# Performance work log

Hardware: AMD Instinct MI355X
Metric: run time of the kernel (lower is better)

## Reference

```python
import jax, jax.numpy as jnp
import numpy as np

S = 2048      # sequence length (q_seq == kv_seq, self-attention)
D = 1024      # hidden_size
H = 16        # num_heads
DH = D // H   # per-head dim
LN_EPS = 1e-5


def setup_inputs() -> dict:
    key = jax.random.key(0)
    ks = jax.random.split(key, 8)
    init = lambda k, shape: (jax.random.normal(k, shape, dtype=jnp.float32)
                             / np.float32(np.sqrt(shape[-1])))
    return {
        "x": jax.random.normal(ks[0], (S, D), dtype=jnp.float32),
        "logit_bias": jax.random.normal(ks[1], (S, H * S), dtype=jnp.float32) * 0.1,
        "mask": jax.random.bernoulli(ks[2], 0.9, (S, S)),
        "Wq": init(ks[3], (D, D)),
        "Wk": init(ks[4], (D, D)),
        "Wv": init(ks[5], (D, D)),
        "Wo": init(ks[6], (D, D)),
        "ln_w": jnp.ones((D,), dtype=jnp.float32),
        "ln_b": jnp.zeros((D,), dtype=jnp.float32),
    }


def reference(x, logit_bias, mask, Wq, Wk, Wv, Wo, ln_w, ln_b):
    # Projections (eqx.nn.Linear: y = W @ x, no bias), split into heads.
    q = (x @ Wq.T).reshape(S, H, DH)  # [s,h,d]
    k = (x @ Wk.T).reshape(S, H, DH)  # [S,h,d]
    v = (x @ Wv.T).reshape(S, H, DH)  # [S,h,d]

    # Scaled scores + per-head additive logit bias.
    scale = jnp.asarray(1.0 / np.sqrt(DH), dtype=q.dtype)
    logits = jnp.einsum('shd,Shd->hsS', q * scale, k)  # [h,s,S]
    logits = logits + logit_bias.reshape(S, H, S).transpose(1, 0, 2)

    # Boolean mask (q_seq, kv_seq) broadcast over heads.
    logits = jnp.where(mask[None, :, :], logits, jnp.finfo(logits.dtype).min)

    # Stable softmax in float32 (matches result_type promotion in source).
    weights = jax.nn.softmax(logits.astype(jnp.float32), axis=-1).astype(logits.dtype)

    attn = jnp.einsum('hsS,Shd->shd', weights, v).reshape(S, D)
    attn_out = attn @ Wo.T  # output projection, no bias

    # Residual + LayerNorm over last dim (eqx.nn.LayerNorm, eps=1e-5).
    res = attn_out + x
    mean = jnp.mean(res, axis=-1, keepdims=True)
    var = jnp.var(res, axis=-1, keepdims=True)
    normed = (res - mean) * jax.lax.rsqrt(var + LN_EPS)
    return normed * ln_w + ln_b
```

## Files before the change

### kernel.cpp

```cpp
#include <hip/hip_runtime.h>

#define SS 2048
#define DD 1024
#define HH 16
#define DHD 64
#define HSN (HH * SS)
#define LOG2E 1.44269504088896340736f

typedef __bf16 bf16x8 __attribute__((ext_vector_type(8)));
typedef __bf16 bf16x4 __attribute__((ext_vector_type(4)));
typedef float f32x4 __attribute__((ext_vector_type(4)));
typedef unsigned int u32;
typedef unsigned long long u64;

__device__ __forceinline__ void glds16(const void* g, void* l) {
  __builtin_amdgcn_global_load_lds(
      (const __attribute__((address_space(1))) u32*)(const u32*)g,
      (__attribute__((address_space(3))) u32*)(u32*)l, 16, 0, 0);
}

__global__ __launch_bounds__(256) void cvt_all_kernel(const float* __restrict__ x,
                                                      const float* __restrict__ Wq,
                                                      const float* __restrict__ Wk,
                                                      const float* __restrict__ Wv,
                                                      const float* __restrict__ Wo,
                                                      __bf16* xb, __bf16* Wqb, __bf16* Wkb,
                                                      __bf16* Wvb, __bf16* Wob) {
  const int z = blockIdx.z;
  const int n4 = (z == 0 ? SS * DD : DD * DD) / 4;
  const int i = blockIdx.x * 256 + threadIdx.x;
  if (i >= n4) return;
  const float* in = z == 0 ? x : (z == 1 ? Wq : (z == 2 ? Wk : (z == 3 ? Wv : Wo)));
  __bf16* out = z == 0 ? xb : (z == 1 ? Wqb : (z == 2 ? Wkb : (z == 3 ? Wvb : Wob)));
  const float4 v = ((const float4*)in)[i];
  bf16x4 r;
  r[0] = (__bf16)v.x; r[1] = (__bf16)v.y; r[2] = (__bf16)v.z; r[3] = (__bf16)v.w;
  *(bf16x4*)&out[(long)i * 4] = r;
}

__global__ __launch_bounds__(256) void pack_mask(const int* __restrict__ mask,
                                                 u64* __restrict__ mp) {
  const long i = (long)blockIdx.x * 256 + threadIdx.x;
  const u64 b = __ballot(mask[i] != 0);
  if ((threadIdx.x & 63) == 0) mp[i >> 6] = b;
}

template <int BM>
__device__ __forceinline__ void gemm_body(const __bf16* __restrict__ A,
                                          const __bf16* __restrict__ B,
                                          void* __restrict__ Cout, float scale, int mode) {
  constexpr int MR = BM / 32;
  __shared__ alignas(16) __bf16 As[BM * 32];
  __shared__ alignas(16) __bf16 Bs[128 * 32];
  const int tid = threadIdx.x;
  const int lane = tid & 63;
  const int wave = tid >> 6;
  const long m0 = (long)blockIdx.y * BM;
  const long n0 = (long)blockIdx.x * 128;
  const int wm = (wave >> 1) * (BM / 2);
  const int wn = (wave & 1) * 64;
  const int g = lane >> 4, r16 = lane & 15;
  const int srow = tid >> 2, sseg = (tid & 3) * 8;

  f32x4 acc[MR][4] = {};

  for (int k0 = 0; k0 < DD; k0 += 32) {
#pragma unroll
    for (int it = 0; it < 2; ++it) {
      const int row = srow + it * 64;
      glds16(&B[(n0 + row) * DD + k0 + sseg], &Bs[row * 32 + sseg]);
    }
#pragma unroll
    for (int it = 0; it < BM / 64; ++it) {
      const int row = srow + it * 64;
      glds16(&A[(m0 + row) * DD + k0 + sseg], &As[row * 32 + sseg]);
    }
    __syncthreads();
    bf16x8 af[MR], bfr[4];
#pragma unroll
    for (int r = 0; r < MR; ++r) af[r] = *(const bf16x8*)&As[(wm + r * 16 + r16) * 32 + g * 8];
#pragma unroll
    for (int c = 0; c < 4; ++c) bfr[c] = *(const bf16x8*)&Bs[(wn + c * 16 + r16) * 32 + g * 8];
#pragma unroll
    for (int r = 0; r < MR; ++r)
#pragma unroll
      for (int c = 0; c < 4; ++c)
        acc[r][c] = __builtin_amdgcn_mfma_f32_16x16x32_bf16(af[r], bfr[c], acc[r][c], 0, 0, 0);
    __syncthreads();
  }

  if (mode == 2) {
#pragma unroll
    for (int r = 0; r < MR; ++r)
#pragma unroll
      for (int c = 0; c < 4; ++c) {
        const long row0 = m0 + wm + r * 16 + g * 4;
        const long col = n0 + wn + c * 16 + r16;
        bf16x4 rv;
#pragma unroll
        for (int i = 0; i < 4; ++i) rv[i] = (__bf16)(acc[r][c][i] * scale);
        *(bf16x4*)&((__bf16*)Cout)[col * SS + row0] = rv;
      }
  } else {
#pragma unroll
    for (int r = 0; r < MR; ++r)
#pragma unroll
      for (int c = 0; c < 4; ++c)
#pragma unroll
        for (int i = 0; i < 4; ++i) {
          const long row = m0 + wm + r * 16 + g * 4 + i;
          const long col = n0 + wn + c * 16 + r16;
          const float v = acc[r][c][i] * scale;
          if (mode == 1) ((float*)Cout)[row * DD + col] = v;
          else           ((__bf16*)Cout)[row * DD + col] = (__bf16)v;
        }
  }
}

__global__ __launch_bounds__(256) void gemm_qkv(const __bf16* __restrict__ A,
                                                const __bf16* __restrict__ B0,
                                                const __bf16* __restrict__ B1,
                                                const __bf16* __restrict__ B2,
                                                __bf16* C0, __bf16* C1, __bf16* C2,
                                                float s0) {
  const int z = blockIdx.z;
  const __bf16* B = z == 0 ? B0 : (z == 1 ? B1 : B2);
  __bf16* C = z == 0 ? C0 : (z == 1 ? C1 : C2);
  gemm_body<128>(A, B, C, z == 0 ? s0 : 1.0f, z == 2 ? 2 : 0);
}

__global__ __launch_bounds__(256) void gemm_o(const __bf16* __restrict__ A,
                                              const __bf16* __restrict__ B,
                                              float* __restrict__ C) {
  gemm_body<64>(A, B, C, 1.0f, 1);
}

__global__ __launch_bounds__(256) void attn_kernel(
    const __bf16* __restrict__ Q, const __bf16* __restrict__ K,
    const __bf16* __restrict__ Vt, const float* __restrict__ bias,
    const u64* __restrict__ mp, __bf16* __restrict__ Aout) {
  __shared__ alignas(16) __bf16 Ks[64][72];
  __shared__ alignas(16) __bf16 Vts[64][72];
  __shared__ alignas(16) __bf16 Ps[4][16][72];
  const int tid = threadIdx.x;
  const int lane = tid & 63;
  const int wave = tid >> 6;
  const int h = blockIdx.y;
  const int q0 = blockIdx.x * 64 + wave * 16;
  const int g = lane >> 4, r16 = lane & 15;
  const int myq = q0 + r16;
  const int srow = tid >> 2;

  bf16x8 qf[2];
#pragma unroll
  for (int c = 0; c < 2; ++c)
    qf[c] = *(const bf16x8*)&Q[(long)myq * DD + h * DHD + c * 32 + g * 8];

  const float* bp = &bias[(long)myq * HSN + h * SS];
  const u64* mrow_p = &mp[(long)myq * (SS / 64)];

  f32x4 o[4] = {};
  float mrow = -__builtin_inff();
  float lsum = 0.f;

  for (int kv0 = 0; kv0 < SS; kv0 += 64) {
    __syncthreads();
#pragma unroll
    for (int it = 0; it < 2; ++it) {
      const int seg = (tid & 3) + it * 4;
      *(bf16x8*)&Ks[srow][seg * 8] =
          *(const bf16x8*)&K[(long)(kv0 + srow) * DD + h * DHD + seg * 8];
      *(bf16x8*)&Vts[srow][seg * 8] =
          *(const bf16x8*)&Vt[(long)(h * DHD + srow) * SS + kv0 + seg * 8];
    }

    float4 bv[4];
#pragma unroll
    for (int t = 0; t < 4; ++t) bv[t] = *(const float4*)&bp[kv0 + t * 16 + g * 4];
    const u64 mw = mrow_p[kv0 >> 6];
    __syncthreads();

    f32x4 s[4];
#pragma unroll
    for (int t = 0; t < 4; ++t) {
      bf16x8 kf0 = *(const bf16x8*)&Ks[t * 16 + r16][g * 8];
      bf16x8 kf1 = *(const bf16x8*)&Ks[t * 16 + r16][32 + g * 8];
      f32x4 acc = {};
      acc = __builtin_amdgcn_mfma_f32_16x16x32_bf16(kf0, qf[0], acc, 0, 0, 0);
      s[t] = __builtin_amdgcn_mfma_f32_16x16x32_bf16(kf1, qf[1], acc, 0, 0, 0);
    }

    float sv[4][4];
#pragma unroll
    for (int t = 0; t < 4; ++t) {
      const u32 mb = (u32)(mw >> (t * 16 + g * 4));
      sv[t][0] = (mb & 1u) ? s[t][0] + bv[t].x * LOG2E : -1e38f;
      sv[t][1] = (mb & 2u) ? s[t][1] + bv[t].y * LOG2E : -1e38f;
      sv[t][2] = (mb & 4u) ? s[t][2] + bv[t].z * LOG2E : -1e38f;
      sv[t][3] = (mb & 8u) ? s[t][3] + bv[t].w * LOG2E : -1e38f;
    }

    float m4 = -1e38f;
#pragma unroll
    for (int t = 0; t < 4; ++t)
#pragma unroll
      for (int i = 0; i < 4; ++i) m4 = fmaxf(m4, sv[t][i]);
    m4 = fmaxf(m4, __shfl_xor(m4, 16));
    m4 = fmaxf(m4, __shfl_xor(m4, 32));
    const float mnew = fmaxf(mrow, m4);
    const float alpha = exp2f(mrow - mnew);
    float ps = 0.f;
    float p[4][4];
#pragma unroll
    for (int t = 0; t < 4; ++t)
#pragma unroll
      for (int i = 0; i < 4; ++i) {
        p[t][i] = exp2f(sv[t][i] - mnew);
        ps += p[t][i];
      }
    ps += __shfl_xor(ps, 16);
    ps += __shfl_xor(ps, 32);
    lsum = lsum * alpha + ps;
    mrow = mnew;
#pragma unroll
    for (int db = 0; db < 4; ++db) o[db] *= alpha;

#pragma unroll
    for (int t = 0; t < 4; ++t) {
      bf16x4 pb;
#pragma unroll
      for (int i = 0; i < 4; ++i) pb[i] = (__bf16)p[t][i];
      *(bf16x4*)&Ps[wave][r16][t * 16 + g * 4] = pb;
    }

#pragma unroll
    for (int kh = 0; kh < 2; ++kh) {
      bf16x8 pf = *(const bf16x8*)&Ps[wave][r16][kh * 32 + g * 8];
#pragma unroll
      for (int db = 0; db < 4; ++db) {
        bf16x8 vf = *(const bf16x8*)&Vts[db * 16 + r16][kh * 32 + g * 8];
        o[db] = __builtin_amdgcn_mfma_f32_16x16x32_bf16(vf, pf, o[db], 0, 0, 0);
      }
    }
  }

  const float rn = 1.f / lsum;
#pragma unroll
  for (int db = 0; db < 4; ++db) {
    bf16x4 r;
#pragma unroll
    for (int i = 0; i < 4; ++i) r[i] = (__bf16)(o[db][i] * rn);
    *(bf16x4*)&Aout[(long)myq * DD + h * DHD + db * 16 + g * 4] = r;
  }
}

__global__ __launch_bounds__(256) void ln_kernel(const float* __restrict__ attn_out,
                                                 const float* __restrict__ x,
                                                 const float* __restrict__ w,
                                                 const float* __restrict__ b,
                                                 float* __restrict__ out) {
  const long row = blockIdx.x;
  const int tid = threadIdx.x;
  float v[4];
  float s = 0.f, s2 = 0.f;
#pragma unroll
  for (int j = 0; j < 4; ++j) {
    const int d = tid + j * 256;
    const float r = attn_out[row * DD + d] + x[row * DD + d];
    v[j] = r; s += r; s2 += r * r;
  }
#pragma unroll
  for (int off = 1; off < 64; off <<= 1) {
    s  += __shfl_xor(s, off);
    s2 += __shfl_xor(s2, off);
  }
  __shared__ float ss[4], ss2[4];
  if ((tid & 63) == 0) { ss[tid >> 6] = s; ss2[tid >> 6] = s2; }
  __syncthreads();
  s = ss[0] + ss[1] + ss[2] + ss[3];
  s2 = ss2[0] + ss2[1] + ss2[2] + ss2[3];
  const float mean = s * (1.f / DD);
  const float var = s2 * (1.f / DD) - mean * mean;
  const float inv = rsqrtf(var + 1e-5f);
#pragma unroll
  for (int j = 0; j < 4; ++j) {
    const int d = tid + j * 256;
    out[row * DD + d] = (v[j] - mean) * inv * w[d] + b[d];
  }
}

extern "C" void kernel_launch(void* const* d_in, const int* in_sizes, int n_in,
                              void* d_out, int out_size, void* d_ws, size_t ws_size,
                              hipStream_t stream) {
  const float* x    = (const float*)d_in[0];
  const float* bias = (const float*)d_in[1];
  const int*   mask = (const int*)d_in[2];
  const float* Wq   = (const float*)d_in[3];
  const float* Wk   = (const float*)d_in[4];
  const float* Wv   = (const float*)d_in[5];
  const float* Wo   = (const float*)d_in[6];
  const float* lnw  = (const float*)d_in[7];
  const float* lnb  = (const float*)d_in[8];
  float* out = (float*)d_out;

  char* ws = (char*)d_ws;
  const size_t MB = 1024 * 1024;
  __bf16* xb   = (__bf16*)(ws + 0);
  __bf16* Wqb  = (__bf16*)(ws + 4 * MB);
  __bf16* Wkb  = (__bf16*)(ws + 6 * MB);
  __bf16* Wvb  = (__bf16*)(ws + 8 * MB);
  __bf16* Wob  = (__bf16*)(ws + 10 * MB);
  __bf16* Qb   = (__bf16*)(ws + 12 * MB);
  __bf16* Kb   = (__bf16*)(ws + 16 * MB);
  __bf16* Vtb  = (__bf16*)(ws + 24 * MB);
  __bf16* Atnb = (__bf16*)(ws + 28 * MB);
  float*  AOut = (float*)(ws + 32 * MB);
  u64*    mpk  = (u64*)(ws + 40 * MB);

  cvt_all_kernel<<<dim3(SS * DD / 1024, 1, 5), dim3(256), 0, stream>>>(
      x, Wq, Wk, Wv, Wo, xb, Wqb, Wkb, Wvb, Wob);

  pack_mask<<<dim3(SS * SS / 256), dim3(256), 0, stream>>>(mask, mpk);

  gemm_qkv<<<dim3(DD / 128, SS / 128, 3), dim3(256), 0, stream>>>(
      xb, Wqb, Wkb, Wvb, Qb, Kb, Vtb, 0.125f * LOG2E);

  attn_kernel<<<dim3(SS / 64, HH), dim3(256), 0, stream>>>(Qb, Kb, Vtb, bias, mpk, Atnb);

  gemm_o<<<dim3(DD / 128, SS / 64), dim3(256), 0, stream>>>(Atnb, Wob, AOut);

  ln_kernel<<<dim3(SS), dim3(256), 0, stream>>>(AOut, x, lnw, lnb, out);
}
```

Before: 488.0 us.

## Widen attention KV tile, remap blocks across XCDs, vectorize layernorm

Attention now processes 128 KV columns per iteration instead of 64, which halves the number of loop iterations and barriers and loads more bias per step. The GEMM and attention kernels remap the flat block index so consecutive blocks spread across the chiplets (XCD-aware swizzle), which is meant to improve L2 locality. The layernorm kernel switches to float4 loads and stores. These changes raise register pressure and LDS use in attention, which may lower occupancy.

```diff
diff --git a/kernel.cpp b/kernel.cpp
--- a/kernel.cpp
+++ b/kernel.cpp
@@ -48,15 +48,16 @@
 template <int BM>
 __device__ __forceinline__ void gemm_body(const __bf16* __restrict__ A,
                                           const __bf16* __restrict__ B,
-                                          void* __restrict__ Cout, float scale, int mode) {
+                                          void* __restrict__ Cout, float scale, int mode,
+                                          int bx, int by) {
   constexpr int MR = BM / 32;
   __shared__ alignas(16) __bf16 As[BM * 32];
   __shared__ alignas(16) __bf16 Bs[128 * 32];
   const int tid = threadIdx.x;
   const int lane = tid & 63;
   const int wave = tid >> 6;
-  const long m0 = (long)blockIdx.y * BM;
-  const long n0 = (long)blockIdx.x * 128;
+  const long m0 = (long)by * BM;
+  const long n0 = (long)bx * 128;
   const int wm = (wave >> 1) * (BM / 2);
   const int wn = (wave & 1) * 64;
   const int g = lane >> 4, r16 = lane & 15;
@@ -123,33 +124,42 @@
                                                 const __bf16* __restrict__ B2,
                                                 __bf16* C0, __bf16* C1, __bf16* C2,
                                                 float s0) {
-  const int z = blockIdx.z;
+  const int flat = blockIdx.x + 8 * (blockIdx.y + 16 * blockIdx.z);
+  const int flat2 = (flat & 7) * 48 + (flat >> 3);
+  const int bx = flat2 & 7;
+  const int t = flat2 >> 3;
+  const int by = t & 15;
+  const int z = t >> 4;
   const __bf16* B = z == 0 ? B0 : (z == 1 ? B1 : B2);
   __bf16* C = z == 0 ? C0 : (z == 1 ? C1 : C2);
-  gemm_body<128>(A, B, C, z == 0 ? s0 : 1.0f, z == 2 ? 2 : 0);
+  gemm_body<128>(A, B, C, z == 0 ? s0 : 1.0f, z == 2 ? 2 : 0, bx, by);
 }
 
 __global__ __launch_bounds__(256) void gemm_o(const __bf16* __restrict__ A,
                                               const __bf16* __restrict__ B,
                                               float* __restrict__ C) {
-  gemm_body<64>(A, B, C, 1.0f, 1);
+  const int flat = blockIdx.x + 8 * blockIdx.y;
+  const int flat2 = (flat & 7) * 32 + (flat >> 3);
+  gemm_body<64>(A, B, C, 1.0f, 1, flat2 & 7, flat2 >> 3);
 }
 
 __global__ __launch_bounds__(256) void attn_kernel(
     const __bf16* __restrict__ Q, const __bf16* __restrict__ K,
     const __bf16* __restrict__ Vt, const float* __restrict__ bias,
     const u64* __restrict__ mp, __bf16* __restrict__ Aout) {
-  __shared__ alignas(16) __bf16 Ks[64][72];
-  __shared__ alignas(16) __bf16 Vts[64][72];
-  __shared__ alignas(16) __bf16 Ps[4][16][72];
+  __shared__ alignas(16) __bf16 Ks[128][72];
+  __shared__ alignas(16) __bf16 Vts[64][136];
+  __shared__ alignas(16) __bf16 Ps[4][16][136];
   const int tid = threadIdx.x;
   const int lane = tid & 63;
   const int wave = tid >> 6;
-  const int h = blockIdx.y;
-  const int q0 = blockIdx.x * 64 + wave * 16;
+  const int flat = blockIdx.x + 32 * blockIdx.y;
+  const int flat2 = (flat & 7) * 64 + (flat >> 3);
+  const int bx = flat2 & 31;
+  const int h = flat2 >> 5;
+  const int q0 = bx * 64 + wave * 16;
   const int g = lane >> 4, r16 = lane & 15;
   const int myq = q0 + r16;
-  const int srow = tid >> 2;
 
   bf16x8 qf[2];
 #pragma unroll
@@ -163,26 +173,30 @@
   float mrow = -__builtin_inff();
   float lsum = 0.f;
 
-  for (int kv0 = 0; kv0 < SS; kv0 += 64) {
+  const int krow = tid >> 1, kcb = (tid & 1) * 4;
+  const int vrow = tid >> 2, vcb = tid & 3;
+
+  for (int kv0 = 0; kv0 < SS; kv0 += 128) {
     __syncthreads();
 #pragma unroll
-    for (int it = 0; it < 2; ++it) {
-      const int seg = (tid & 3) + it * 4;
-      *(bf16x8*)&Ks[srow][seg * 8] =
-          *(const bf16x8*)&K[(long)(kv0 + srow) * DD + h * DHD + seg * 8];
-      *(bf16x8*)&Vts[srow][seg * 8] =
-          *(const bf16x8*)&Vt[(long)(h * DHD + srow) * SS + kv0 + seg * 8];
-    }
-
-    float4 bv[4];
-#pragma unroll
-    for (int t = 0; t < 4; ++t) bv[t] = *(const float4*)&bp[kv0 + t * 16 + g * 4];
-    const u64 mw = mrow_p[kv0 >> 6];
+    for (int it = 0; it < 4; ++it)
+      *(bf16x8*)&Ks[krow][(kcb + it) * 8] =
+          *(const bf16x8*)&K[(long)(kv0 + krow) * DD + h * DHD + (kcb + it) * 8];
+#pragma unroll
+    for (int it = 0; it < 4; ++it)
+      *(bf16x8*)&Vts[vrow][(vcb + it * 4) * 8] =
+          *(const bf16x8*)&Vt[(long)(h * DHD + vrow) * SS + kv0 + (vcb + it * 4) * 8];
+
+    float4 bv[8];
+#pragma unroll
+    for (int t = 0; t < 8; ++t) bv[t] = *(const float4*)&bp[kv0 + t * 16 + g * 4];
+    const u64 mwA = mrow_p[kv0 >> 6];
+    const u64 mwB = mrow_p[(kv0 >> 6) + 1];
     __syncthreads();
 
-    f32x4 s[4];
-#pragma unroll
-    for (int t = 0; t < 4; ++t) {
+    f32x4 s[8];
+#pragma unroll
+    for (int t = 0; t < 8; ++t) {
       bf16x8 kf0 = *(const bf16x8*)&Ks[t * 16 + r16][g * 8];
       bf16x8 kf1 = *(const bf16x8*)&Ks[t * 16 + r16][32 + g * 8];
       f32x4 acc = {};
@@ -190,33 +204,32 @@
       s[t] = __builtin_amdgcn_mfma_f32_16x16x32_bf16(kf1, qf[1], acc, 0, 0, 0);
     }
 
-    float sv[4][4];
-#pragma unroll
-    for (int t = 0; t < 4; ++t) {
-      const u32 mb = (u32)(mw >> (t * 16 + g * 4));
-      sv[t][0] = (mb & 1u) ? s[t][0] + bv[t].x * LOG2E : -1e38f;
-      sv[t][1] = (mb & 2u) ? s[t][1] + bv[t].y * LOG2E : -1e38f;
-      sv[t][2] = (mb & 4u) ? s[t][2] + bv[t].z * LOG2E : -1e38f;
-      sv[t][3] = (mb & 8u) ? s[t][3] + bv[t].w * LOG2E : -1e38f;
+    float l[8][4];
+#pragma unroll
+    for (int t = 0; t < 8; ++t) {
+      const u32 mb = (u32)((t < 4 ? mwA : mwB) >> ((t & 3) * 16 + g * 4));
+      l[t][0] = (mb & 1u) ? s[t][0] + bv[t].x * LOG2E : -1e38f;
+      l[t][1] = (mb & 2u) ? s[t][1] + bv[t].y * LOG2E : -1e38f;
+      l[t][2] = (mb & 4u) ? s[t][2] + bv[t].z * LOG2E : -1e38f;
+      l[t][3] = (mb & 8u) ? s[t][3] + bv[t].w * LOG2E : -1e38f;
     }
 
     float m4 = -1e38f;
 #pragma unroll
-    for (int t = 0; t < 4; ++t)
-#pragma unroll
-      for (int i = 0; i < 4; ++i) m4 = fmaxf(m4, sv[t][i]);
+    for (int t = 0; t < 8; ++t)
+#pragma unroll
+      for (int i = 0; i < 4; ++i) m4 = fmaxf(m4, l[t][i]);
     m4 = fmaxf(m4, __shfl_xor(m4, 16));
     m4 = fmaxf(m4, __shfl_xor(m4, 32));
     const float mnew = fmaxf(mrow, m4);
     const float alpha = exp2f(mrow - mnew);
     float ps = 0.f;
-    float p[4][4];
-#pragma unroll
-    for (int t = 0; t < 4; ++t)
+#pragma unroll
+    for (int t = 0; t < 8; ++t)
 #pragma unroll
       for (int i = 0; i < 4; ++i) {
-        p[t][i] = exp2f(sv[t][i] - mnew);
-        ps += p[t][i];
+        l[t][i] = exp2f(l[t][i] - mnew);
+        ps += l[t][i];
       }
     ps += __shfl_xor(ps, 16);
     ps += __shfl_xor(ps, 32);
@@ -226,15 +239,15 @@
     for (int db = 0; db < 4; ++db) o[db] *= alpha;
 
 #pragma unroll
-    for (int t = 0; t < 4; ++t) {
+    for (int t = 0; t < 8; ++t) {
       bf16x4 pb;
 #pragma unroll
-      for (int i = 0; i < 4; ++i) pb[i] = (__bf16)p[t][i];
+      for (int i = 0; i < 4; ++i) pb[i] = (__bf16)l[t][i];
       *(bf16x4*)&Ps[wave][r16][t * 16 + g * 4] = pb;
     }
 
 #pragma unroll
-    for (int kh = 0; kh < 2; ++kh) {
+    for (int kh = 0; kh < 4; ++kh) {
       bf16x8 pf = *(const bf16x8*)&Ps[wave][r16][kh * 32 + g * 8];
 #pragma unroll
       for (int db = 0; db < 4; ++db) {
@@ -261,14 +274,12 @@
                                                  float* __restrict__ out) {
   const long row = blockIdx.x;
   const int tid = threadIdx.x;
-  float v[4];
+  const float4 a4 = ((const float4*)&attn_out[row * DD])[tid];
+  const float4 x4 = ((const float4*)&x[row * DD])[tid];
+  float v[4] = {a4.x + x4.x, a4.y + x4.y, a4.z + x4.z, a4.w + x4.w};
   float s = 0.f, s2 = 0.f;
 #pragma unroll
-  for (int j = 0; j < 4; ++j) {
-    const int d = tid + j * 256;
-    const float r = attn_out[row * DD + d] + x[row * DD + d];
-    v[j] = r; s += r; s2 += r * r;
-  }
+  for (int j = 0; j < 4; ++j) { s += v[j]; s2 += v[j] * v[j]; }
 #pragma unroll
   for (int off = 1; off < 64; off <<= 1) {
     s  += __shfl_xor(s, off);
@@ -282,11 +293,14 @@
   const float mean = s * (1.f / DD);
   const float var = s2 * (1.f / DD) - mean * mean;
   const float inv = rsqrtf(var + 1e-5f);
-#pragma unroll
-  for (int j = 0; j < 4; ++j) {
-    const int d = tid + j * 256;
-    out[row * DD + d] = (v[j] - mean) * inv * w[d] + b[d];
-  }
+  const float4 w4 = ((const float4*)w)[tid];
+  const float4 b4 = ((const float4*)b)[tid];
+  float4 o4;
+  o4.x = (v[0] - mean) * inv * w4.x + b4.x;
+  o4.y = (v[1] - mean) * inv * w4.y + b4.y;
+  o4.z = (v[2] - mean) * inv * w4.z + b4.z;
+  o4.w = (v[3] - mean) * inv * w4.w + b4.w;
+  ((float4*)&out[row * DD])[tid] = o4;
 }
 
 extern "C" void kernel_launch(void* const* d_in, const int* in_sizes, int n_in,
```

New measurement: 506.3 us. 3.8% more time.
